# Kernel optimization log

Hardware: AMD Instinct MI355X
Metric: run time of the kernel (lower is better)

The kernel has to match this reference:

```python
import jax, jax.numpy as jnp
import numpy as np

B, L, E, H, V, ENC = 64, 51, 512, 512, 30000, 2048


def setup_inputs() -> dict:
    key = jax.random.key(0)
    ks = jax.random.split(key, 12)
    encoder_out = jax.random.normal(ks[0], (B, ENC), jnp.float32)
    encoded_captions = jax.random.randint(ks[1], (B, L), 0, V)
    lengths = jax.random.randint(ks[2], (B,), 2, L + 1)
    lengths = lengths.at[0].set(L)  # ensure max(decode_lengths) == L-1 so T is static
    caption_lengths = lengths[:, None]

    def lin(k, out_d, in_d):
        bnd = 1.0 / np.sqrt(in_d)
        kw, kb = jax.random.split(k)
        w = jax.random.uniform(kw, (out_d, in_d), jnp.float32, -bnd, bnd)
        b = jax.random.uniform(kb, (out_d,), jnp.float32, -bnd, bnd)
        return w, b

    embedding_weight = jax.random.uniform(ks[3], (V, E), jnp.float32, -0.1, 0.1)
    w_ih, b_ih = lin(ks[4], 4 * H, E)
    w_hh, b_hh = lin(ks[5], 4 * H, H)
    w_init_h, b_init_h = lin(ks[6], H, ENC)
    w_init_c, b_init_c = lin(ks[7], H, ENC)
    w_fc = jax.random.uniform(ks[8], (V, H), jnp.float32, -0.1, 0.1)
    b_fc = jnp.zeros((V,), jnp.float32)
    return dict(encoder_out=encoder_out, encoded_captions=encoded_captions,
                caption_lengths=caption_lengths, embedding_weight=embedding_weight,
                w_ih=w_ih, b_ih=b_ih, w_hh=w_hh, b_hh=b_hh,
                w_init_h=w_init_h, b_init_h=b_init_h,
                w_init_c=w_init_c, b_init_c=b_init_c, w_fc=w_fc, b_fc=b_fc)


def _forward(encoder_out, embedding_weight, w_ih, b_ih, w_hh, b_hh,
             w_init_h, b_init_h, w_init_c, b_init_c, w_fc, b_fc,
             encoded_captions, caption_lengths):
    lengths = caption_lengths[:, 0]
    sort_ind = jnp.argsort(-lengths)          # descending-length sort
    enc = encoder_out[sort_ind]
    caps = encoded_captions[sort_ind]
    dec_len = lengths[sort_ind] - 1           # [B]
    embs = embedding_weight[caps]             # [B, L, E]
    h0 = enc @ w_init_h.T + b_init_h          # [B, H]
    c0 = enc @ w_init_c.T + b_init_c
    T = caps.shape[1] - 1                     # static max(decode_lengths)
    xs = (jnp.transpose(embs[:, :T], (1, 0, 2)), jnp.arange(T))

    # Note: the torch loop trims h,c to batch_size_t; because lengths are
    # sorted descending, trimmed rows never produce outputs again, so running
    # the full batch and masking finished rows yields identical predictions.
    def step(carry, xt):
        h, c = carry
        x, t = xt
        gates = x @ w_ih.T + b_ih + h @ w_hh.T + b_hh   # [B, 4H]
        i, f, g, o = jnp.split(gates, 4, axis=-1)       # LSTMCell gate order
        c = jax.nn.sigmoid(f) * c + jax.nn.sigmoid(i) * jnp.tanh(g)
        h = jax.nn.sigmoid(o) * jnp.tanh(c)
        preds = h @ w_fc.T + b_fc                        # dropout = identity (eval)
        preds = jnp.where((t < dec_len)[:, None], preds, 0.0)
        return (h, c), preds

    _, preds = jax.lax.scan(step, (h0, c0), xs)          # [T, B, V]
    predictions = jnp.transpose(preds, (1, 0, 2))        # [B, T, V]
    return predictions, caps, dec_len, sort_ind


def reference(encoder_out, encoded_captions, caption_lengths, embedding_weight,
              w_ih, b_ih, w_hh, b_hh, w_init_h, b_init_h, w_init_c, b_init_c,
              w_fc, b_fc):
    return _forward(encoder_out, embedding_weight, w_ih, b_ih, w_hh, b_hh,
                    w_init_h, b_init_h, w_init_c, b_init_c, w_fc, b_fc,
                    encoded_captions, caption_lengths)
```

## Files before the change

kernel.cpp:

```cpp
#include <hip/hip_runtime.h>

#define NB    64
#define LCAP  51
#define TT    50
#define HID   512
#define EMB   512
#define VOC   30000
#define ENCD  2048
#define G4    2048

typedef unsigned short u16;
typedef unsigned int   u32;
typedef __attribute__((ext_vector_type(8))) short bf16x8;
typedef __attribute__((ext_vector_type(4))) float f32x4;
typedef __attribute__((ext_vector_type(4))) unsigned int u32x4;

__device__ __forceinline__ u16 f2bf(float x) {
  union { float f; unsigned u; } v; v.f = x;
  unsigned r = v.u + 0x7fffu + ((v.u >> 16) & 1u);
  return (u16)(r >> 16);
}

__device__ __forceinline__ float fast_sigmoid(float x) {
  return 1.f / (1.f + __expf(-x));
}
__device__ __forceinline__ float fast_tanh(float x) {
  float xx = fminf(fmaxf(x, -10.f), 10.f);
  float e = __expf(2.f * xx);
  return (e - 1.f) * __frcp_rn(e + 1.f);
}

template <int SLEEP>
__device__ __forceinline__ void poll_flags16(const int* flg, int lane, u32 tt) {
  if (lane < 16) {
    const u32* myp = (const u32*)flg + lane;
    u32 f;
    for (;;) {
      asm volatile("global_load_dword %0, %1, off sc0 sc1"
                   : "=v"(f) : "v"(myp) : "memory");
      asm volatile("s_waitcnt vmcnt(0)" : "+v"(f) :: "memory");
      if (((f & 0xffu) >= tt) & (((f >> 8) & 0xffu) >= tt) &
          (((f >> 16) & 0xffu) >= tt) & ((f >> 24) >= tt)) break;
      __builtin_amdgcn_s_sleep(SLEEP);
    }
  }
}

__global__ __launch_bounds__(256) void sort_k(const int* __restrict__ cap_len,
                                              const int* __restrict__ caps,
                                              float* __restrict__ out,
                                              int* __restrict__ sind,
                                              int* __restrict__ dlen,
                                              int* __restrict__ trow,
                                              int* __restrict__ zmap,
                                              int* __restrict__ nact,
                                              int* __restrict__ flags,
                                              int* __restrict__ tileneed) {
  __shared__ int smlen[NB];
  __shared__ int smpos[NB];
  __shared__ int sdl[NB];
  __shared__ int cnt_s[TT];
  __shared__ int toff_s[TT];
  __shared__ int trow_s[NB * TT];
  int tid = threadIdx.x;
  if (tid < NB) { smlen[tid] = cap_len[tid]; flags[tid] = 0; }
  __syncthreads();
  if (tid < NB) {
    int li = smlen[tid];
    int rank = 0;
    for (int j = 0; j < NB; ++j) {
      int lj = smlen[j];
      rank += (lj > li || (lj == li && j < tid)) ? 1 : 0;
    }
    smpos[rank] = tid;
  }
  __syncthreads();
  if (tid < NB) {
    int src = smpos[tid];
    int dl = smlen[src] - 1;
    sind[tid] = src;
    dlen[tid] = dl;
    sdl[tid] = dl;
    float* caps_out = out + (size_t)NB * TT * VOC;
    for (int l = 0; l < LCAP; ++l)
      caps_out[tid * LCAP + l] = (float)caps[src * LCAP + l];
    out[96003264 + tid] = (float)dl;
    out[96003328 + tid] = (float)src;
  }
  __syncthreads();
  if (tid < TT) {
    int c = 0;
    for (int b = 0; b < NB; ++b) c += (sdl[b] > tid) ? 1 : 0;
    cnt_s[tid] = c;
  }
  __syncthreads();
  if (tid == 0) {
    int s = 0;
    for (int t = 0; t < TT; ++t) { toff_s[t] = s; s += cnt_s[t]; }
    *nact = s;
  }
  __syncthreads();
  if (tid < TT) {
    int t = tid;
    int o = toff_s[t];
    int z = t * NB - o;
    int c = cnt_s[t];
    for (int b = 0; b < NB; ++b) {
      int m = b * TT + t;
      if (b < c) trow_s[o + b] = m;
      else       zmap[z + (b - c)] = m;
    }
  }
  __syncthreads();
  int na = toff_s[TT - 1] + cnt_s[TT - 1];
  for (int k = tid; k < na; k += 256) trow[k] = trow_s[k];
  if (tid < 25) {
    int i = tid;
    if (i * 128 < na) {
      int k = min(i * 128 + 127, na - 1);
      tileneed[i] = (trow_s[k] % TT) + 2;
    }
  }
}

__global__ __launch_bounds__(256) void prep_k(const float* __restrict__ w_ih,
                                              const float* __restrict__ wh,
                                              const float* __restrict__ wc,
                                              const float* __restrict__ enc,
                                              const float* __restrict__ emb,
                                              const int* __restrict__ caps,
                                              const int* __restrict__ sind,
                                              u16* __restrict__ Wih,
                                              u16* __restrict__ Winit,
                                              u16* __restrict__ Ebf,
                                              u16* __restrict__ Xb) {
  int i = blockIdx.x * 256 + threadIdx.x;
  const float* src;
  u16* dstp;
  if (i < 262144) {
    src = w_ih + (size_t)i * 4;
    dstp = Wih + (size_t)i * 4;
  } else if (i < 786432) {
    int e = (i - 262144) * 4;
    int row = e >> 11, col = e & 2047;
    src = (row < 512) ? (wh + (size_t)row * 2048 + col)
                      : (wc + (size_t)(row - 512) * 2048 + col);
    dstp = Winit + (size_t)(i - 262144) * 4;
  } else if (i < 819200) {
    int e = (i - 786432) * 4;
    int r = e >> 11, k = e & 2047;
    src = enc + (size_t)sind[r] * ENCD + k;
    dstp = Ebf + (size_t)(i - 786432) * 4;
  } else if (i < 1228800) {
    int e = (i - 819200) * 4;
    int m = e >> 9, k = e & 511;
    unsigned b = ((unsigned)m * 5243u) >> 18;
    int t = m - (int)b * TT;
    int cap = caps[sind[b] * LCAP + t];
    src = emb + (size_t)cap * EMB + k;
    dstp = Xb + (size_t)(i - 819200) * 4;
  } else return;
  float4 v = *(const float4*)src;
  ushort4 o;
  o.x = f2bf(v.x); o.y = f2bf(v.y); o.z = f2bf(v.z); o.w = f2bf(v.w);
  *(ushort4*)dstp = o;
}

#define BM 128
#define BN 128
#define BK 32
#define LDT 40

template <int EPI>
__global__ __launch_bounds__(256) void gemm_bt(const u16* __restrict__ A,
                                               const u16* __restrict__ Bm,
                                               int Mr, int Nr, int K,
                                               void* __restrict__ outv,
                                               float* __restrict__ out1,
                                               const float* __restrict__ bias0,
                                               const float* __restrict__ bias1) {
  __shared__ u16 As[BM * LDT];
  __shared__ u16 Bs[BN * LDT];
  int tid = threadIdx.x;
  int mBase = blockIdx.x * BM;
  int nBase = blockIdx.y * BN;

  int wid = tid >> 6, lane = tid & 63;
  int wm = (wid >> 1) * 64, wn = (wid & 1) * 64;
  int lm = lane & 15, lq = lane >> 4;

  f32x4 acc[4][4];
  for (int i = 0; i < 4; ++i)
    for (int j = 0; j < 4; ++j)
      acc[i][j] = (f32x4){0.f, 0.f, 0.f, 0.f};

  int nkt = K / BK;
  for (int kt = 0; kt < nkt; ++kt) {
    for (int it = 0; it < 2; ++it) {
      int li = tid + it * 256;
      int row = li >> 2, kq = li & 3;
      {
        int gr = min(mBase + row, Mr - 1);
        uint4 v = *(const uint4*)(A + (size_t)gr * K + kt * BK + kq * 8);
        *(uint4*)&As[row * LDT + kq * 8] = v;
      }
      {
        int gr = min(nBase + row, Nr - 1);
        uint4 v = *(const uint4*)(Bm + (size_t)gr * K + kt * BK + kq * 8);
        *(uint4*)&Bs[row * LDT + kq * 8] = v;
      }
    }
    __syncthreads();
    bf16x8 af[4], bfr[4];
    for (int i = 0; i < 4; ++i)
      af[i] = *(const bf16x8*)&As[(wm + i * 16 + lm) * LDT + lq * 8];
    for (int j = 0; j < 4; ++j)
      bfr[j] = *(const bf16x8*)&Bs[(wn + j * 16 + lm) * LDT + lq * 8];
    for (int i = 0; i < 4; ++i)
      for (int j = 0; j < 4; ++j)
        acc[i][j] = __builtin_amdgcn_mfma_f32_16x16x32_bf16(af[i], bfr[j], acc[i][j], 0, 0, 0);
    __syncthreads();
  }

  for (int i = 0; i < 4; ++i) {
    int rloc0 = wm + i * 16 + (lane >> 4) * 4;
    for (int j = 0; j < 4; ++j) {
      int col = nBase + wn + j * 16 + (lane & 15);
      for (int r = 0; r < 4; ++r) {
        int rloc = rloc0 + r;
        float v = acc[i][j][r];
        if (EPI == 0) {
          int row = mBase + rloc;
          if (row < Mr && col < Nr)
            ((float*)outv)[(size_t)row * Nr + col] = v + bias0[col] + bias1[col];
        } else {
          int row = mBase + rloc;
          if (row < Mr && col < Nr) {
            if (col < 512) {
              int jj = col >> 3;
              ((u16*)outv)[(size_t)jj * 512 + row * 8 + (col & 7)] = f2bf(v + bias0[col]);
            } else {
              out1[(size_t)row * 512 + (col - 512)] = v + bias1[col - 512];
            }
          }
        }
      }
    }
  }
}

__global__ __launch_bounds__(256, 1) void lstm_fc(const float* __restrict__ w_hh,
                                                  const float* __restrict__ xW,
                                                  const float* __restrict__ cbuf,
                                                  u32* __restrict__ hx,
                                                  u32* __restrict__ Hs32,
                                                  int* __restrict__ flg,
                                                  const float* __restrict__ w_fc,
                                                  u16* __restrict__ Wfc,
                                                  const float* __restrict__ b_fc,
                                                  const int* __restrict__ trow,
                                                  const int* __restrict__ zmap,
                                                  const int* __restrict__ nactp,
                                                  const int* __restrict__ tileneed,
                                                  float* __restrict__ out) {
  __shared__ __align__(16) char smem[43520];
  int tid = threadIdx.x;
  int wave = tid >> 6, lane = tid & 63;
  int lm = lane & 15, lq = lane >> 4;

  if (blockIdx.x < 64) {
    u16* wsm = (u16*)smem;
    float* gsmf = (float*)(smem + 33280);
    u32* hsh = (u32*)(smem + 33280 + 9216);
#define GSM(rr, cc) gsmf[(rr) * 36 + (cc)]
    int j = blockIdx.x;
    int u0 = j * 8;

    {
      int r = tid >> 3;
      int cc = (tid & 7) * 64;
      const float* src = w_hh + (size_t)((r >> 3) * HID + u0 + (r & 7)) * HID + cc;
      u16* dst = &wsm[r * 520 + cc];
#pragma unroll
      for (int q = 0; q < 16; ++q) {
        float4 v = ((const float4*)src)[q];
        ushort4 o; o.x = f2bf(v.x); o.y = f2bf(v.y); o.z = f2bf(v.z); o.w = f2bf(v.w);
        ((ushort4*)dst)[q] = o;
      }
    }
    __syncthreads();

    bf16x8 bfrag[2][16];
#pragma unroll
    for (int n = 0; n < 2; ++n)
#pragma unroll
      for (int kq = 0; kq < 16; ++kq)
        bfrag[n][kq] = *(const bf16x8*)&wsm[(n * 16 + lm) * 520 + kq * 32 + lq * 8];

    int b = tid >> 2, up = tid & 3;
    float creg[2];
    {
      float2 c2 = *(const float2*)&cbuf[(size_t)b * HID + u0 + 2 * up];
      creg[0] = c2.x; creg[1] = c2.y;
    }

    const int abase = lq * 256 + (wave * 16 + lm) * 4;

    for (int t = 0; t < TT; ++t) {
      const u32* hcur = hx + (size_t)(t & 1) * (NB * 256);
      u32* hnxt = hx + (size_t)((t + 1) & 1) * (NB * 256);

      float xg[4][2];
      {
        const float* xwp = xW + (size_t)(b * TT + t) * G4 + u0 + 2 * up;
#pragma unroll
        for (int g = 0; g < 4; ++g) {
          float2 v = *(const float2*)&xwp[g * HID];
          xg[g][0] = v.x; xg[g][1] = v.y;
        }
      }

      if (t > 0) {
        if (wave == 0) poll_flags16<1>(flg, lane, (u32)t);
        __syncthreads();
      }

      u32x4 raw[16];
#pragma unroll
      for (int kq = 0; kq < 16; ++kq) {
        const u32* p = hcur + abase + kq * 1024;
        asm volatile("global_load_dwordx4 %0, %1, off sc0 sc1"
                     : "=v"(raw[kq]) : "v"(p) : "memory");
      }
      asm volatile("s_waitcnt vmcnt(0)"
                   : "+v"(raw[0]), "+v"(raw[1]), "+v"(raw[2]), "+v"(raw[3]),
                     "+v"(raw[4]), "+v"(raw[5]), "+v"(raw[6]), "+v"(raw[7]),
                     "+v"(raw[8]), "+v"(raw[9]), "+v"(raw[10]), "+v"(raw[11]),
                     "+v"(raw[12]), "+v"(raw[13]), "+v"(raw[14]), "+v"(raw[15])
                   :: "memory");

      f32x4 acc0 = (f32x4){0.f, 0.f, 0.f, 0.f};
      f32x4 acc1 = (f32x4){0.f, 0.f, 0.f, 0.f};
#pragma unroll
      for (int kq = 0; kq < 16; ++kq) {
        bf16x8 a = __builtin_bit_cast(bf16x8, raw[kq]);
        acc0 = __builtin_amdgcn_mfma_f32_16x16x32_bf16(a, bfrag[0][kq], acc0, 0, 0, 0);
        acc1 = __builtin_amdgcn_mfma_f32_16x16x32_bf16(a, bfrag[1][kq], acc1, 0, 0, 0);
      }
#pragma unroll
      for (int r = 0; r < 4; ++r) {
        GSM(wave * 16 + lq * 4 + r, lm)      = acc0[r];
        GSM(wave * 16 + lq * 4 + r, 16 + lm) = acc1[r];
      }

      float hn2[2];
#pragma unroll
      for (int e = 0; e < 2; ++e) {
        int ul = 2 * up + e;
        float gi = GSM(b, ul)      + xg[0][e];
        float gf = GSM(b, 8 + ul)  + xg[1][e];
        float gg = GSM(b, 16 + ul) + xg[2][e];
        float go = GSM(b, 24 + ul) + xg[3][e];
        float cn = fast_sigmoid(gf) * creg[e] + fast_sigmoid(gi) * fast_tanh(gg);
        creg[e] = cn;
        hn2[e] = fast_sigmoid(go) * fast_tanh(cn);
      }
      hsh[b * 4 + up] = (u32)f2bf(hn2[0]) | ((u32)f2bf(hn2[1]) << 16);
      __syncthreads();

      if (tid < 64) {
        u32x4 hv = *(const u32x4*)&hsh[tid * 4];
        u32* dst = hnxt + j * 256 + tid * 4;
        asm volatile("global_store_dwordx4 %0, %1, off sc0 sc1"
                     :: "v"(dst), "v"(hv) : "memory");
        asm volatile("s_waitcnt vmcnt(0)" ::: "memory");
        if (tid == 0) {
          u32 fv = (u32)(t + 1);
          unsigned char* fj = (unsigned char*)flg + j;
          asm volatile("global_store_byte %0, %1, off sc0 sc1"
                       :: "v"(fj), "v"(fv) : "memory");
        }
        u32* hdst = Hs32 + ((size_t)tid * TT + t) * 256 + j * 4;
        asm volatile("global_store_dwordx4 %0, %1, off sc0 sc1"
                     :: "v"(hdst), "v"(hv) : "memory");
      }
    }
    if (wave == 0) {
      asm volatile("s_waitcnt vmcnt(0)" ::: "memory");
      if (lane == 0) {
        u32 fv = 51u;
        unsigned char* fj = (unsigned char*)flg + j;
        asm volatile("global_store_byte %0, %1, off sc0 sc1"
                     :: "v"(fj), "v"(fv) : "memory");
      }
    }
#undef GSM
  } else {
    u16* As = (u16*)smem;
    u16* Bs = (u16*)(smem + 10240);
    int* rmap_s = (int*)(smem + 20480);
    int* tn_s = (int*)(smem + 20992);
    const u16* HsA = (const u16*)Hs32;

    if (tid < 25) tn_s[tid] = tileneed[tid];
    int nactv = nactp[0];
    int ntiles = (nactv + 127) >> 7;
    int totjobs = ntiles * 235;
    __syncthreads();

    const int F = 192;
    int f = blockIdx.x - 64;
    int fs = (f & 7) * 24 + (f >> 3);
    int per = (totjobs + F - 1) / F;
    int J0 = fs * per;
    int J1 = min(J0 + per, totjobs);
    int wm = (wave >> 1) * 64, wn = (wave & 1) * 64;

    if (J0 < J1) {
      int p0 = J0 / ntiles, p1 = (J1 - 1) / ntiles;

      for (int p = p0; p <= p1; ++p) {
        int r0 = p * 128;
        int r1 = min(r0 + 128, VOC);
        int nel4 = (r1 - r0) * 128;
        const float4* src = (const float4*)(w_fc + (size_t)r0 * 512);
        ushort4* dst = (ushort4*)(Wfc + (size_t)r0 * 512);
        for (int i = tid; i < nel4; i += 256) {
          float4 v = src[i];
          ushort4 o;
          o.x = f2bf(v.x); o.y = f2bf(v.y); o.z = f2bf(v.z); o.w = f2bf(v.w);
          dst[i] = o;
        }
      }
      __syncthreads();

      int lastNeed = 0;
      for (int rt = 0; rt < ntiles; ++rt) {
        int need = tn_s[rt];
        bool any = false;
        for (int p = p0; p <= p1; ++p) {
          int J = p * ntiles + rt;
          if (J >= J0 && J < J1) { any = true; break; }
        }
        if (!any) continue;
        if (need > lastNeed) {
          if (wave == 0) poll_flags16<64>(flg, lane, (u32)need);
          lastNeed = need;
        }
        __syncthreads();
        if (tid < 128) {
          int k = (rt << 7) + tid;
          rmap_s[tid] = trow[(k < nactv) ? k : (nactv - 1)];
        }
        __syncthreads();

        for (int p = p0; p <= p1; ++p) {
          int J = p * ntiles + rt;
          if (J < J0 || J >= J1) continue;
          int nBase = p * 128;

          f32x4 acc[4][4];
          for (int i = 0; i < 4; ++i)
            for (int jj = 0; jj < 4; ++jj)
              acc[i][jj] = (f32x4){0.f, 0.f, 0.f, 0.f};

          for (int kt = 0; kt < 16; ++kt) {
            for (int it = 0; it < 2; ++it) {
              int li = tid + it * 256;
              int row = li >> 2, kq = li & 3;
              {
                int gr = rmap_s[row];
                uint4 v = *(const uint4*)(HsA + (size_t)gr * 512 + kt * BK + kq * 8);
                *(uint4*)&As[row * LDT + kq * 8] = v;
              }
              {
                int gb = min(nBase + row, VOC - 1);
                uint4 v = *(const uint4*)(Wfc + (size_t)gb * 512 + kt * BK + kq * 8);
                *(uint4*)&Bs[row * LDT + kq * 8] = v;
              }
            }
            __syncthreads();
            bf16x8 af[4], bfr[4];
            for (int i = 0; i < 4; ++i)
              af[i] = *(const bf16x8*)&As[(wm + i * 16 + lm) * LDT + lq * 8];
            for (int jj = 0; jj < 4; ++jj)
              bfr[jj] = *(const bf16x8*)&Bs[(wn + jj * 16 + lm) * LDT + lq * 8];
            for (int i = 0; i < 4; ++i)
              for (int jj = 0; jj < 4; ++jj)
                acc[i][jj] = __builtin_amdgcn_mfma_f32_16x16x32_bf16(af[i], bfr[jj], acc[i][jj], 0, 0, 0);
            __syncthreads();
          }

          for (int i = 0; i < 4; ++i) {
            int rloc0 = wm + i * 16 + lq * 4;
            for (int jj = 0; jj < 4; ++jj) {
              int col = nBase + wn + jj * 16 + lm;
              if (col < VOC) {
                float bias = b_fc[col];
                for (int r = 0; r < 4; ++r) {
                  int m = rmap_s[rloc0 + r];
                  out[(size_t)m * VOC + col] = acc[i][jj][r] + bias;
                }
              }
            }
          }
        }
      }
    }

    int nz = NB * TT - nactv;
    float4 zz = {0.f, 0.f, 0.f, 0.f};
    for (int r = f; r < nz; r += F) {
      float4* dst = (float4*)(out + (size_t)zmap[r] * VOC);
      for (int c4 = tid; c4 < VOC / 4; c4 += 256) dst[c4] = zz;
    }
  }
}

extern "C" void kernel_launch(void* const* d_in, const int* in_sizes, int n_in,
                              void* d_out, int out_size, void* d_ws, size_t ws_size,
                              hipStream_t stream) {
  const float* encoder_out = (const float*)d_in[0];
  const int*   caps        = (const int*)d_in[1];
  const int*   cap_len     = (const int*)d_in[2];
  const float* emb         = (const float*)d_in[3];
  const float* w_ih        = (const float*)d_in[4];
  const float* b_ih        = (const float*)d_in[5];
  const float* w_hh        = (const float*)d_in[6];
  const float* b_hh        = (const float*)d_in[7];
  const float* w_init_h    = (const float*)d_in[8];
  const float* b_init_h    = (const float*)d_in[9];
  const float* w_init_c    = (const float*)d_in[10];
  const float* b_init_c    = (const float*)d_in[11];
  const float* w_fc        = (const float*)d_in[12];
  const float* b_fc        = (const float*)d_in[13];
  float* out = (float*)d_out;

  char* ws = (char*)d_ws;
  int*   sind    = (int*)(ws + 0);
  int*   dlen    = (int*)(ws + 256);
  int*   nact    = (int*)(ws + 512);
  int*   flags   = (int*)(ws + 576);
  int*   tilend  = (int*)(ws + 640);
  int*   trow    = (int*)(ws + 832);
  int*   zmap    = (int*)(ws + 13632);
  float* cbuf    = (float*)(ws + 26496);
  u16*   hbuf    = (u16*)(ws + 157568);
  float* xW      = (float*)(ws + 288640);
  u16*   Hs      = (u16*)(ws + 26503040);
  u16*   Xb      = (u16*)(ws + 29779840);
  u16*   Wih     = (u16*)(ws + 33056640);
  u16*   Winit   = (u16*)(ws + 35153792);
  u16*   Wfc     = (u16*)(ws + 39348096);
  u16*   Ebf     = (u16*)(ws + 70068096);

  sort_k<<<1, 256, 0, stream>>>(cap_len, caps, out, sind, dlen, trow, zmap,
                                nact, flags, tilend);
  prep_k<<<4800, 256, 0, stream>>>(w_ih, w_init_h, w_init_c, encoder_out,
                                   emb, caps, sind, Wih, Winit, Ebf, Xb);

  gemm_bt<1><<<dim3(1, 8), 256, 0, stream>>>(Ebf, Winit, 64, 1024, 2048,
                                             hbuf, cbuf, b_init_h, b_init_c);
  gemm_bt<0><<<dim3(25, 16), 256, 0, stream>>>(Xb, Wih, 3200, 2048, 512,
                                               xW, nullptr, b_ih, b_hh);
  lstm_fc<<<256, 256, 0, stream>>>(w_hh, xW, cbuf, (u32*)hbuf, (u32*)Hs, flags,
                                   w_fc, Wfc, b_fc, trow, zmap, nact, tilend, out);
}
```

Before: 859.8 us.

## Move w_fc bf16 conversion into prep kernel and relayout hidden-state history

The fp32-to-bf16 conversion of the 30000x512 output projection weight moves out of the FC worker blocks of the persistent LSTM kernel and into the prep kernel, which now runs with many more blocks. The saved hidden-state history is also stored in a time-major, k-chunked layout, and the FC blocks precompute per-row offsets into it. The aim is to take conversion work off the FC blocks' critical path and make the hidden-state writes and A-tile loads more contiguous. The cost is a longer serial prep phase before the recurrence starts, where the conversion previously overlapped with it.

```diff
diff --git a/kernel.cpp b/kernel.cpp
--- a/kernel.cpp
+++ b/kernel.cpp
@@ -128,12 +128,14 @@
                                               const float* __restrict__ wc,
                                               const float* __restrict__ enc,
                                               const float* __restrict__ emb,
+                                              const float* __restrict__ w_fc,
                                               const int* __restrict__ caps,
                                               const int* __restrict__ sind,
                                               u16* __restrict__ Wih,
                                               u16* __restrict__ Winit,
                                               u16* __restrict__ Ebf,
-                                              u16* __restrict__ Xb) {
+                                              u16* __restrict__ Xb,
+                                              u16* __restrict__ Wfc) {
   int i = blockIdx.x * 256 + threadIdx.x;
   const float* src;
   u16* dstp;
@@ -159,6 +161,10 @@
     int cap = caps[sind[b] * LCAP + t];
     src = emb + (size_t)cap * EMB + k;
     dstp = Xb + (size_t)(i - 819200) * 4;
+  } else if (i < 5068800) {
+    size_t idx = (size_t)(i - 1228800) * 4;
+    src = w_fc + idx;
+    dstp = Wfc + idx;
   } else return;
   float4 v = *(const float4*)src;
   ushort4 o;
@@ -255,8 +261,7 @@
                                                   u32* __restrict__ hx,
                                                   u32* __restrict__ Hs32,
                                                   int* __restrict__ flg,
-                                                  const float* __restrict__ w_fc,
-                                                  u16* __restrict__ Wfc,
+                                                  const u16* __restrict__ Wfc,
                                                   const float* __restrict__ b_fc,
                                                   const int* __restrict__ trow,
                                                   const int* __restrict__ zmap,
@@ -380,7 +385,7 @@
           asm volatile("global_store_byte %0, %1, off sc0 sc1"
                        :: "v"(fj), "v"(fv) : "memory");
         }
-        u32* hdst = Hs32 + ((size_t)tid * TT + t) * 256 + j * 4;
+        u32* hdst = Hs32 + (size_t)t * 16384 + j * 256 + tid * 4;
         asm volatile("global_store_dwordx4 %0, %1, off sc0 sc1"
                      :: "v"(hdst), "v"(hv) : "memory");
       }
@@ -399,8 +404,9 @@
     u16* As = (u16*)smem;
     u16* Bs = (u16*)(smem + 10240);
     int* rmap_s = (int*)(smem + 20480);
-    int* tn_s = (int*)(smem + 20992);
-    const u16* HsA = (const u16*)Hs32;
+    int* hsl_s = (int*)(smem + 20992);
+    int* tn_s = (int*)(smem + 21504);
+    const u16* HsU = (const u16*)Hs32;
 
     if (tid < 25) tn_s[tid] = tileneed[tid];
     int nactv = nactp[0];
@@ -419,21 +425,6 @@
     if (J0 < J1) {
       int p0 = J0 / ntiles, p1 = (J1 - 1) / ntiles;
 
-      for (int p = p0; p <= p1; ++p) {
-        int r0 = p * 128;
-        int r1 = min(r0 + 128, VOC);
-        int nel4 = (r1 - r0) * 128;
-        const float4* src = (const float4*)(w_fc + (size_t)r0 * 512);
-        ushort4* dst = (ushort4*)(Wfc + (size_t)r0 * 512);
-        for (int i = tid; i < nel4; i += 256) {
-          float4 v = src[i];
-          ushort4 o;
-          o.x = f2bf(v.x); o.y = f2bf(v.y); o.z = f2bf(v.z); o.w = f2bf(v.w);
-          dst[i] = o;
-        }
-      }
-      __syncthreads();
-
       int lastNeed = 0;
       for (int rt = 0; rt < ntiles; ++rt) {
         int need = tn_s[rt];
@@ -450,7 +441,11 @@
         __syncthreads();
         if (tid < 128) {
           int k = (rt << 7) + tid;
-          rmap_s[tid] = trow[(k < nactv) ? k : (nactv - 1)];
+          int m = trow[(k < nactv) ? k : (nactv - 1)];
+          int bb = (m * 5243) >> 18;
+          int tt = m - bb * TT;
+          rmap_s[tid] = m;
+          hsl_s[tid] = tt * 32768 + bb * 8;
         }
         __syncthreads();
 
@@ -469,8 +464,7 @@
               int li = tid + it * 256;
               int row = li >> 2, kq = li & 3;
               {
-                int gr = rmap_s[row];
-                uint4 v = *(const uint4*)(HsA + (size_t)gr * 512 + kt * BK + kq * 8);
+                uint4 v = *(const uint4*)(HsU + (size_t)hsl_s[row] + (kt * 4 + kq) * 512);
                 *(uint4*)&As[row * LDT + kq * 8] = v;
               }
               {
@@ -556,13 +550,14 @@
 
   sort_k<<<1, 256, 0, stream>>>(cap_len, caps, out, sind, dlen, trow, zmap,
                                 nact, flags, tilend);
-  prep_k<<<4800, 256, 0, stream>>>(w_ih, w_init_h, w_init_c, encoder_out,
-                                   emb, caps, sind, Wih, Winit, Ebf, Xb);
+  prep_k<<<19800, 256, 0, stream>>>(w_ih, w_init_h, w_init_c, encoder_out,
+                                    emb, w_fc, caps, sind,
+                                    Wih, Winit, Ebf, Xb, Wfc);
 
   gemm_bt<1><<<dim3(1, 8), 256, 0, stream>>>(Ebf, Winit, 64, 1024, 2048,
                                              hbuf, cbuf, b_init_h, b_init_c);
   gemm_bt<0><<<dim3(25, 16), 256, 0, stream>>>(Xb, Wih, 3200, 2048, 512,
                                                xW, nullptr, b_ih, b_hh);
   lstm_fc<<<256, 256, 0, stream>>>(w_hh, xW, cbuf, (u32*)hbuf, (u32*)Hs, flags,
-                                   w_fc, Wfc, b_fc, trow, zmap, nact, tilend, out);
-}
+                                   Wfc, b_fc, trow, zmap, nact, tilend, out);
+}
```

Result: slower. 901.7 us (+4.9%).
